# Kernel tuning notes

Hardware: AMD Instinct MI355X
Metric: run time of the kernel (lower is better)

Reference implementation:

```python
import jax, jax.numpy as jnp
import numpy as np

N_NODES = 50000
N_EDGES = 1600000
IN_FEAT, H_FEAT, OUT_FEAT, N_CLASSES = 256, 128, 64, 8


def setup_inputs() -> dict:
    key = jax.random.key(0)
    ks = jax.random.split(key, 8)
    seq = jax.random.normal(ks[0], (N_NODES, IN_FEAT), dtype=jnp.float32)
    edge_index = jax.random.randint(ks[1], (2, N_EDGES), 0, N_NODES, dtype=jnp.int64)
    # GCNConv weights (stored as [in, out]) and biases; Glorot-ish scale
    W1 = jax.random.normal(ks[2], (IN_FEAT, H_FEAT), dtype=jnp.float32) / np.sqrt(IN_FEAT)
    b1 = jnp.zeros((H_FEAT,), dtype=jnp.float32)
    W2 = jax.random.normal(ks[3], (H_FEAT, OUT_FEAT), dtype=jnp.float32) / np.sqrt(H_FEAT)
    b2 = jnp.zeros((OUT_FEAT,), dtype=jnp.float32)
    Wc = jax.random.normal(ks[4], (OUT_FEAT, N_CLASSES), dtype=jnp.float32) / np.sqrt(OUT_FEAT)
    bc = jnp.zeros((N_CLASSES,), dtype=jnp.float32)
    return {"seq": seq, "edge_index": edge_index,
            "W1": W1, "b1": b1, "W2": W2, "b2": b2, "Wc": Wc, "bc": bc}


def _gcn_conv(x, W, b, src, dst, norm, n_nodes):
    # PyG GCNConv: h = x @ W, then symmetric-normalized aggregation to dst, + bias
    h = x @ W                                   # [N, out]
    msg = h[src] * norm[:, None]                # [E+N, out] gather + scale
    out = jax.ops.segment_sum(msg, dst, num_segments=n_nodes)  # scatter-add
    return out + b


def reference(seq, edge_index, W1, b1, W2, b2, Wc, bc):
    n = seq.shape[0]
    loops = jnp.arange(n, dtype=edge_index.dtype)
    src = jnp.concatenate([edge_index[0], loops])  # add self-loops
    dst = jnp.concatenate([edge_index[1], loops])
    # symmetric normalization deg^{-1/2}[src] * deg^{-1/2}[dst]
    deg = jax.ops.segment_sum(jnp.ones_like(dst, dtype=seq.dtype), dst, num_segments=n)
    dinv = jnp.where(deg > 0, jax.lax.rsqrt(deg), 0.0)
    norm = dinv[src] * dinv[dst]                  # [E+N]
    res1 = _gcn_conv(seq, W1, b1, src, dst, norm, n)
    res2 = _gcn_conv(res1, W2, b2, src, dst, norm, n)
    return res2 @ Wc + bc
```

## Files before the change

kernel.cpp:

```cpp
#include <hip/hip_runtime.h>
#include <hip/hip_bf16.h>
#include <stdint.h>

#define NN 50000
#define NE 1600000
#define BSH 7
#define NBK 391
#define CAP 4608
#define NSB 256
#define ECH 6250

__global__ __launch_bounds__(256) void k_wcombo(const float* __restrict__ W1, const float* __restrict__ b1,
                                                const float* __restrict__ W2, const float* __restrict__ b2,
                                                const float* __restrict__ Wc, const float* __restrict__ bc,
                                                float* __restrict__ Wcombo, float* __restrict__ c12){
  __shared__ float M1[128 * 8];
  int t = threadIdx.x;
  for (int idx = t; idx < 1024; idx += 256){
    int k = idx >> 3, c = idx & 7;
    float s = 0.f;
    for (int j = 0; j < 64; ++j) s += W2[k * 64 + j] * Wc[j * 8 + c];
    M1[idx] = s;
  }
  __syncthreads();
  if (blockIdx.x < 8){
    int i = blockIdx.x * 32 + (t >> 3), c = t & 7;
    float s = 0.f;
    for (int k = 0; k < 128; ++k) s += W1[i * 128 + k] * M1[k * 8 + c];
    Wcombo[i * 8 + c] = s;
  } else {
    if (t < 8){
      float s = 0.f;
      for (int k = 0; k < 128; ++k) s += b1[k] * M1[k * 8 + t];
      c12[t] = s;
    } else if (t < 16){
      int c = t - 8;
      float s = bc[c];
      for (int k = 0; k < 64; ++k) s += b2[k] * Wc[k * 8 + c];
      c12[t] = s;
    }
  }
}

__global__ __launch_bounds__(256) void k_hist(const int* __restrict__ dst, int* __restrict__ bh){
  __shared__ int h[4 * NBK];
  for (int i = threadIdx.x; i < 4 * NBK; i += 256) h[i] = 0;
  __syncthreads();
  const int wv = (threadIdx.x >> 6) * NBK;
  const int e0 = blockIdx.x * ECH;
  for (int e = e0 + threadIdx.x; e < e0 + ECH; e += 256)
    atomicAdd(&h[wv + (dst[e] >> BSH)], 1);
  __syncthreads();
  for (int i = threadIdx.x; i < NBK; i += 256)
    bh[(size_t)blockIdx.x * NBK + i] = h[i] + h[NBK + i] + h[2 * NBK + i] + h[3 * NBK + i];
}

__global__ __launch_bounds__(NSB) void k_bscan(const int* __restrict__ bh, int* __restrict__ boff,
                                               int* __restrict__ btot){
  __shared__ int lds[NSB];
  const int b = blockIdx.x;
  int v = bh[(size_t)threadIdx.x * NBK + b];
  lds[threadIdx.x] = v;
  __syncthreads();
  for (int ofs = 1; ofs < NSB; ofs <<= 1){
    int t = (threadIdx.x >= ofs) ? lds[threadIdx.x - ofs] : 0;
    __syncthreads();
    lds[threadIdx.x] += t;
    __syncthreads();
  }
  boff[(size_t)threadIdx.x * NBK + b] = lds[threadIdx.x] - v;
  if (threadIdx.x == NSB - 1) btot[b] = lds[NSB - 1];
}

__global__ __launch_bounds__(256) void k_scat(const int* __restrict__ src, const int* __restrict__ dst,
                                              const int* __restrict__ boff, uint32_t* __restrict__ ebuf){
  __shared__ int ctr[NBK];
  for (int i = threadIdx.x; i < NBK; i += 256)
    ctr[i] = i * CAP + boff[(size_t)blockIdx.x * NBK + i];
  __syncthreads();
  const int e0 = blockIdx.x * ECH;
  for (int e = e0 + threadIdx.x; e < e0 + ECH; e += 256){
    int d = dst[e];
    int s = src[e];
    int p = atomicAdd(&ctr[d >> BSH], 1);
    ebuf[p] = ((uint32_t)s << 16) | (uint32_t)d;
  }
}

__global__ __launch_bounds__(256) void k_csr(const uint32_t* __restrict__ ebuf, const int* __restrict__ btot,
                                             float* __restrict__ dinv, int2* __restrict__ offs2,
                                             unsigned short* __restrict__ csr){
  __shared__ uint32_t lede[CAP];
  __shared__ unsigned short lcsr[CAP];
  __shared__ int h[128];
  __shared__ int sb[128];
  const int t = threadIdx.x;
  const int b = blockIdx.x;
  const int base = b * CAP;
  const int cnt = btot[b];
  for (int i = t; i < cnt; i += 256) lede[i] = ebuf[base + i];
  if (t < 128) h[t] = 0;
  __syncthreads();
  for (int i = t; i < cnt; i += 256)
    atomicAdd(&h[lede[i] & 127], 1);
  __syncthreads();
  int deg = (t < 128) ? h[t] : 0;
  for (int ofs = 1; ofs < 128; ofs <<= 1){
    int tv = (t >= ofs && t < 128) ? h[t - ofs] : 0;
    __syncthreads();
    if (t < 128) h[t] += tv;
    __syncthreads();
  }
  int excl = (t < 128) ? (h[t] - deg) : 0;
  int node = (b << BSH) + t;
  if (t < 128 && node < NN){
    dinv[node] = rsqrtf((float)(deg + 1));
    offs2[node] = make_int2(base + excl, base + excl + deg);
  }
  __syncthreads();
  if (t < 128) sb[t] = excl;
  __syncthreads();
  for (int i = t; i < cnt; i += 256){
    uint32_t v = lede[i];
    int p = atomicAdd(&sb[v & 127], 1);
    lcsr[p] = (unsigned short)(v >> 16);
  }
  __syncthreads();
  uint32_t* dstw = (uint32_t*)(csr + base);
  const uint32_t* srcw = (const uint32_t*)lcsr;
  int nw = (cnt + 1) >> 1;
  for (int i = t; i < nw; i += 256) dstw[i] = srcw[i];
}

__global__ __launch_bounds__(256) void k_y(const float* __restrict__ X, const float* __restrict__ Wcombo,
                                           const float* __restrict__ dinv, float* __restrict__ Yp){
  __shared__ float Wl[2048];
  int t = threadIdx.x;
  for (int i = t; i < 2048; i += 256) Wl[i] = Wcombo[i];
  __syncthreads();
  int gid = blockIdx.x * 256 + t;
  int row = gid >> 3, c = gid & 7;
  if (row >= NN) return;
  const float* Xr = X + (size_t)row * 256;
  float acc = 0.f;
  #pragma unroll 8
  for (int k = 0; k < 256; k += 4){
    float4 x = *(const float4*)(Xr + k);
    acc += x.x * Wl[k * 8 + c] + x.y * Wl[(k + 1) * 8 + c]
         + x.z * Wl[(k + 2) * 8 + c] + x.w * Wl[(k + 3) * 8 + c];
  }
  Yp[(size_t)row * 8 + c] = acc * dinv[row];
}

__global__ __launch_bounds__(256) void k_agg1(const unsigned short* __restrict__ csr, const int2* __restrict__ offs2,
                                              const float* __restrict__ dinv, const float* __restrict__ Yp,
                                              float* __restrict__ U, float* __restrict__ V){
  int gid = blockIdx.x * 256 + threadIdx.x;
  int node = gid >> 3, c = gid & 7;
  if (node >= NN) return;
  int2 oe = offs2[node];
  int e = oe.x;
  const int e1 = oe.y;
  float a = 0.f, vd = 0.f;
  for (; e + 4 <= e1; e += 4){
    int s0 = csr[e], s1 = csr[e + 1], s2 = csr[e + 2], s3 = csr[e + 3];
    float y0 = Yp[(size_t)s0 * 8 + c], y1 = Yp[(size_t)s1 * 8 + c];
    float y2 = Yp[(size_t)s2 * 8 + c], y3 = Yp[(size_t)s3 * 8 + c];
    a += (y0 + y1) + (y2 + y3);
    if (c == 0) vd += (dinv[s0] + dinv[s1]) + (dinv[s2] + dinv[s3]);
  }
  for (; e < e1; ++e){
    int s0 = csr[e];
    a += Yp[(size_t)s0 * 8 + c];
    if (c == 0) vd += dinv[s0];
  }
  float di = dinv[node];
  U[(size_t)node * 8 + c] = di * di * (a + Yp[(size_t)node * 8 + c]);
  if (c == 0) V[node] = di * (vd + di);
}

__global__ __launch_bounds__(256) void k_agg2(const unsigned short* __restrict__ csr, const int2* __restrict__ offs2,
                                              const float* __restrict__ dinv, const float* __restrict__ U,
                                              const float* __restrict__ V, const float* __restrict__ c12,
                                              float* __restrict__ O){
  int gid = blockIdx.x * 256 + threadIdx.x;
  int node = gid >> 3, c = gid & 7;
  if (node >= NN) return;
  int2 oe = offs2[node];
  int e = oe.x;
  const int e1 = oe.y;
  float a = 0.f;
  for (; e + 4 <= e1; e += 4){
    int s0 = csr[e], s1 = csr[e + 1], s2 = csr[e + 2], s3 = csr[e + 3];
    float y0 = U[(size_t)s0 * 8 + c], y1 = U[(size_t)s1 * 8 + c];
    float y2 = U[(size_t)s2 * 8 + c], y3 = U[(size_t)s3 * 8 + c];
    a += (y0 + y1) + (y2 + y3);
  }
  for (; e < e1; ++e){
    int s0 = csr[e];
    a += U[(size_t)s0 * 8 + c];
  }
  float di = dinv[node];
  O[(size_t)node * 8 + c] = di * (a + U[(size_t)node * 8 + c]) + V[node] * c12[c] + c12[8 + c];
}

extern "C" void kernel_launch(void* const* d_in, const int* in_sizes, int n_in,
                              void* d_out, int out_size, void* d_ws, size_t ws_size,
                              hipStream_t stream) {
  const float* seq = (const float*)d_in[0];
  const int*   ei  = (const int*)d_in[1];
  const int*   esrc = ei;
  const int*   edst = ei + NE;
  const float* W1 = (const float*)d_in[2];
  const float* b1 = (const float*)d_in[3];
  const float* W2 = (const float*)d_in[4];
  const float* b2 = (const float*)d_in[5];
  const float* Wc = (const float*)d_in[6];
  const float* bc = (const float*)d_in[7];
  float* out = (float*)d_out;

  char* ws = (char*)d_ws;
  size_t o = 0;
  auto alloc = [&](size_t bytes) -> void* {
    void* p = ws + o;
    o += (bytes + 255) & ~(size_t)255;
    return p;
  };
  int*      bh    = (int*)alloc((size_t)NSB * NBK * 4);
  int*      boff  = (int*)alloc((size_t)NSB * NBK * 4);
  int*      btot  = (int*)alloc((size_t)NBK * 4);
  uint32_t* ebuf  = (uint32_t*)alloc((size_t)NBK * CAP * 4);
  unsigned short* csr = (unsigned short*)alloc((size_t)NBK * CAP * 2);
  int2*     offs2 = (int2*)alloc((size_t)NN * 8);
  float*    dinv  = (float*)alloc((size_t)NN * 4);
  float*    Wcb   = (float*)alloc(2048 * 4);
  float*    c12   = (float*)alloc(16 * 4);
  float*    Yp    = (float*)alloc((size_t)NN * 8 * 4);
  float*    U     = (float*)alloc((size_t)NN * 8 * 4);
  float*    V     = (float*)alloc((size_t)NN * 4);

  k_wcombo <<<9, 256, 0, stream>>>(W1, b1, W2, b2, Wc, bc, Wcb, c12);
  k_hist   <<<NSB, 256, 0, stream>>>(edst, bh);
  k_bscan  <<<NBK, NSB, 0, stream>>>(bh, boff, btot);
  k_scat   <<<NSB, 256, 0, stream>>>(esrc, edst, boff, ebuf);
  k_csr    <<<NBK, 256, 0, stream>>>(ebuf, btot, dinv, offs2, csr);
  k_y      <<<(NN * 8 + 255) / 256, 256, 0, stream>>>(seq, Wcb, dinv, Yp);
  k_agg1   <<<(NN * 8 + 255) / 256, 256, 0, stream>>>(csr, offs2, dinv, Yp, U, V);
  k_agg2   <<<(NN * 8 + 255) / 256, 256, 0, stream>>>(csr, offs2, dinv, U, V, c12, out);
}
```

Measured before the change: 99.25 us.

## Merge independent kernels horizontally and move dinv scaling of Y into aggregation

The weight-combination kernel now shares one launch with the destination histogram, and the edge scatter shares one launch with the X·Wcombo projection. Because the projection no longer depends on dinv, it can run before the CSR build, and the source-side dinv scaling moves into agg1 as a per-edge multiply. This cuts two launches and lets the 51 MB read of X overlap with the scatter. In exchange agg1 does an extra dinv gather and multiply per edge in every lane, not just lane 0.

```diff
diff --git a/kernel.cpp b/kernel.cpp
--- a/kernel.cpp
+++ b/kernel.cpp
@@ -9,50 +9,53 @@
 #define CAP 4608
 #define NSB 256
 #define ECH 6250
-
-__global__ __launch_bounds__(256) void k_wcombo(const float* __restrict__ W1, const float* __restrict__ b1,
-                                                const float* __restrict__ W2, const float* __restrict__ b2,
-                                                const float* __restrict__ Wc, const float* __restrict__ bc,
-                                                float* __restrict__ Wcombo, float* __restrict__ c12){
+#define NYB 1563
+
+__global__ __launch_bounds__(256) void k_iw(const float* __restrict__ W1, const float* __restrict__ b1,
+                                            const float* __restrict__ W2, const float* __restrict__ b2,
+                                            const float* __restrict__ Wc, const float* __restrict__ bc,
+                                            float* __restrict__ Wcombo, float* __restrict__ c12,
+                                            const int* __restrict__ dst, int* __restrict__ bh){
   __shared__ float M1[128 * 8];
-  int t = threadIdx.x;
-  for (int idx = t; idx < 1024; idx += 256){
-    int k = idx >> 3, c = idx & 7;
-    float s = 0.f;
-    for (int j = 0; j < 64; ++j) s += W2[k * 64 + j] * Wc[j * 8 + c];
-    M1[idx] = s;
-  }
-  __syncthreads();
-  if (blockIdx.x < 8){
-    int i = blockIdx.x * 32 + (t >> 3), c = t & 7;
-    float s = 0.f;
-    for (int k = 0; k < 128; ++k) s += W1[i * 128 + k] * M1[k * 8 + c];
-    Wcombo[i * 8 + c] = s;
+  __shared__ int h[4 * NBK];
+  const int t = threadIdx.x;
+  if (blockIdx.x < 9){
+    for (int idx = t; idx < 1024; idx += 256){
+      int k = idx >> 3, c = idx & 7;
+      float s = 0.f;
+      for (int j = 0; j < 64; ++j) s += W2[k * 64 + j] * Wc[j * 8 + c];
+      M1[idx] = s;
+    }
+    __syncthreads();
+    if (blockIdx.x < 8){
+      int i = blockIdx.x * 32 + (t >> 3), c = t & 7;
+      float s = 0.f;
+      for (int k = 0; k < 128; ++k) s += W1[i * 128 + k] * M1[k * 8 + c];
+      Wcombo[i * 8 + c] = s;
+    } else {
+      if (t < 8){
+        float s = 0.f;
+        for (int k = 0; k < 128; ++k) s += b1[k] * M1[k * 8 + t];
+        c12[t] = s;
+      } else if (t < 16){
+        int c = t - 8;
+        float s = bc[c];
+        for (int k = 0; k < 64; ++k) s += b2[k] * Wc[k * 8 + c];
+        c12[t] = s;
+      }
+    }
   } else {
-    if (t < 8){
-      float s = 0.f;
-      for (int k = 0; k < 128; ++k) s += b1[k] * M1[k * 8 + t];
-      c12[t] = s;
-    } else if (t < 16){
-      int c = t - 8;
-      float s = bc[c];
-      for (int k = 0; k < 64; ++k) s += b2[k] * Wc[k * 8 + c];
-      c12[t] = s;
-    }
-  }
-}
-
-__global__ __launch_bounds__(256) void k_hist(const int* __restrict__ dst, int* __restrict__ bh){
-  __shared__ int h[4 * NBK];
-  for (int i = threadIdx.x; i < 4 * NBK; i += 256) h[i] = 0;
-  __syncthreads();
-  const int wv = (threadIdx.x >> 6) * NBK;
-  const int e0 = blockIdx.x * ECH;
-  for (int e = e0 + threadIdx.x; e < e0 + ECH; e += 256)
-    atomicAdd(&h[wv + (dst[e] >> BSH)], 1);
-  __syncthreads();
-  for (int i = threadIdx.x; i < NBK; i += 256)
-    bh[(size_t)blockIdx.x * NBK + i] = h[i] + h[NBK + i] + h[2 * NBK + i] + h[3 * NBK + i];
+    const int hb = blockIdx.x - 9;
+    for (int i = t; i < 4 * NBK; i += 256) h[i] = 0;
+    __syncthreads();
+    const int wv = (t >> 6) * NBK;
+    const int e0 = hb * ECH;
+    for (int e = e0 + t; e < e0 + ECH; e += 256)
+      atomicAdd(&h[wv + (dst[e] >> BSH)], 1);
+    __syncthreads();
+    for (int i = t; i < NBK; i += 256)
+      bh[(size_t)hb * NBK + i] = h[i] + h[NBK + i] + h[2 * NBK + i] + h[3 * NBK + i];
+  }
 }
 
 __global__ __launch_bounds__(NSB) void k_bscan(const int* __restrict__ bh, int* __restrict__ boff,
@@ -72,18 +75,39 @@
   if (threadIdx.x == NSB - 1) btot[b] = lds[NSB - 1];
 }
 
-__global__ __launch_bounds__(256) void k_scat(const int* __restrict__ src, const int* __restrict__ dst,
-                                              const int* __restrict__ boff, uint32_t* __restrict__ ebuf){
+__global__ __launch_bounds__(256) void k_sy(const int* __restrict__ src, const int* __restrict__ dst,
+                                            const int* __restrict__ boff, uint32_t* __restrict__ ebuf,
+                                            const float* __restrict__ X, const float* __restrict__ Wcombo,
+                                            float* __restrict__ Yraw){
   __shared__ int ctr[NBK];
-  for (int i = threadIdx.x; i < NBK; i += 256)
-    ctr[i] = i * CAP + boff[(size_t)blockIdx.x * NBK + i];
-  __syncthreads();
-  const int e0 = blockIdx.x * ECH;
-  for (int e = e0 + threadIdx.x; e < e0 + ECH; e += 256){
-    int d = dst[e];
-    int s = src[e];
-    int p = atomicAdd(&ctr[d >> BSH], 1);
-    ebuf[p] = ((uint32_t)s << 16) | (uint32_t)d;
+  __shared__ float Wl[2048];
+  const int t = threadIdx.x;
+  if (blockIdx.x < NSB){
+    for (int i = t; i < NBK; i += 256)
+      ctr[i] = i * CAP + boff[(size_t)blockIdx.x * NBK + i];
+    __syncthreads();
+    const int e0 = blockIdx.x * ECH;
+    for (int e = e0 + t; e < e0 + ECH; e += 256){
+      int d = dst[e];
+      int s = src[e];
+      int p = atomicAdd(&ctr[d >> BSH], 1);
+      ebuf[p] = ((uint32_t)s << 16) | (uint32_t)d;
+    }
+  } else {
+    for (int i = t; i < 2048; i += 256) Wl[i] = Wcombo[i];
+    __syncthreads();
+    int gid = (blockIdx.x - NSB) * 256 + t;
+    int row = gid >> 3, c = gid & 7;
+    if (row >= NN) return;
+    const float* Xr = X + (size_t)row * 256;
+    float acc = 0.f;
+    #pragma unroll 8
+    for (int k = 0; k < 256; k += 4){
+      float4 x = *(const float4*)(Xr + k);
+      acc += x.x * Wl[k * 8 + c] + x.y * Wl[(k + 1) * 8 + c]
+           + x.z * Wl[(k + 2) * 8 + c] + x.w * Wl[(k + 3) * 8 + c];
+    }
+    Yraw[(size_t)row * 8 + c] = acc;
   }
 }
 
@@ -132,28 +156,8 @@
   for (int i = t; i < nw; i += 256) dstw[i] = srcw[i];
 }
 
-__global__ __launch_bounds__(256) void k_y(const float* __restrict__ X, const float* __restrict__ Wcombo,
-                                           const float* __restrict__ dinv, float* __restrict__ Yp){
-  __shared__ float Wl[2048];
-  int t = threadIdx.x;
-  for (int i = t; i < 2048; i += 256) Wl[i] = Wcombo[i];
-  __syncthreads();
-  int gid = blockIdx.x * 256 + t;
-  int row = gid >> 3, c = gid & 7;
-  if (row >= NN) return;
-  const float* Xr = X + (size_t)row * 256;
-  float acc = 0.f;
-  #pragma unroll 8
-  for (int k = 0; k < 256; k += 4){
-    float4 x = *(const float4*)(Xr + k);
-    acc += x.x * Wl[k * 8 + c] + x.y * Wl[(k + 1) * 8 + c]
-         + x.z * Wl[(k + 2) * 8 + c] + x.w * Wl[(k + 3) * 8 + c];
-  }
-  Yp[(size_t)row * 8 + c] = acc * dinv[row];
-}
-
 __global__ __launch_bounds__(256) void k_agg1(const unsigned short* __restrict__ csr, const int2* __restrict__ offs2,
-                                              const float* __restrict__ dinv, const float* __restrict__ Yp,
+                                              const float* __restrict__ dinv, const float* __restrict__ Y,
                                               float* __restrict__ U, float* __restrict__ V){
   int gid = blockIdx.x * 256 + threadIdx.x;
   int node = gid >> 3, c = gid & 7;
@@ -164,18 +168,20 @@
   float a = 0.f, vd = 0.f;
   for (; e + 4 <= e1; e += 4){
     int s0 = csr[e], s1 = csr[e + 1], s2 = csr[e + 2], s3 = csr[e + 3];
-    float y0 = Yp[(size_t)s0 * 8 + c], y1 = Yp[(size_t)s1 * 8 + c];
-    float y2 = Yp[(size_t)s2 * 8 + c], y3 = Yp[(size_t)s3 * 8 + c];
-    a += (y0 + y1) + (y2 + y3);
-    if (c == 0) vd += (dinv[s0] + dinv[s1]) + (dinv[s2] + dinv[s3]);
+    float d0 = dinv[s0], d1 = dinv[s1], d2 = dinv[s2], d3 = dinv[s3];
+    float y0 = Y[(size_t)s0 * 8 + c], y1 = Y[(size_t)s1 * 8 + c];
+    float y2 = Y[(size_t)s2 * 8 + c], y3 = Y[(size_t)s3 * 8 + c];
+    a += (d0 * y0 + d1 * y1) + (d2 * y2 + d3 * y3);
+    vd += (d0 + d1) + (d2 + d3);
   }
   for (; e < e1; ++e){
     int s0 = csr[e];
-    a += Yp[(size_t)s0 * 8 + c];
-    if (c == 0) vd += dinv[s0];
+    float d0 = dinv[s0];
+    a += d0 * Y[(size_t)s0 * 8 + c];
+    vd += d0;
   }
   float di = dinv[node];
-  U[(size_t)node * 8 + c] = di * di * (a + Yp[(size_t)node * 8 + c]);
+  U[(size_t)node * 8 + c] = di * di * (a + di * Y[(size_t)node * 8 + c]);
   if (c == 0) V[node] = di * (vd + di);
 }
 
@@ -235,16 +241,14 @@
   float*    dinv  = (float*)alloc((size_t)NN * 4);
   float*    Wcb   = (float*)alloc(2048 * 4);
   float*    c12   = (float*)alloc(16 * 4);
-  float*    Yp    = (float*)alloc((size_t)NN * 8 * 4);
+  float*    Yraw  = (float*)alloc((size_t)NN * 8 * 4);
   float*    U     = (float*)alloc((size_t)NN * 8 * 4);
   float*    V     = (float*)alloc((size_t)NN * 4);
 
-  k_wcombo <<<9, 256, 0, stream>>>(W1, b1, W2, b2, Wc, bc, Wcb, c12);
-  k_hist   <<<NSB, 256, 0, stream>>>(edst, bh);
+  k_iw     <<<9 + NSB, 256, 0, stream>>>(W1, b1, W2, b2, Wc, bc, Wcb, c12, edst, bh);
   k_bscan  <<<NBK, NSB, 0, stream>>>(bh, boff, btot);
-  k_scat   <<<NSB, 256, 0, stream>>>(esrc, edst, boff, ebuf);
+  k_sy     <<<NSB + NYB, 256, 0, stream>>>(esrc, edst, boff, ebuf, seq, Wcb, Yraw);
   k_csr    <<<NBK, 256, 0, stream>>>(ebuf, btot, dinv, offs2, csr);
-  k_y      <<<(NN * 8 + 255) / 256, 256, 0, stream>>>(seq, Wcb, dinv, Yp);
-  k_agg1   <<<(NN * 8 + 255) / 256, 256, 0, stream>>>(csr, offs2, dinv, Yp, U, V);
-  k_agg2   <<<(NN * 8 + 255) / 256, 256, 0, stream>>>(csr, offs2, dinv, U, V, c12, out);
-}
+  k_agg1   <<<NYB, 256, 0, stream>>>(csr, offs2, dinv, Yraw, U, V);
+  k_agg2   <<<NYB, 256, 0, stream>>>(csr, offs2, dinv, U, V, c12, out);
+}
```

New measurement: 88.90 us. 1.12x faster.
